# Performance work log

Measured on AMD Instinct MI355X. Metric: run time of the kernel, lower is better.

## Reference

```python
import jax, jax.numpy as jnp
import numpy as np

N_CLUSTERS = 16
N_ITERATIONS = 5
COV_INIT = 1.0


def setup_inputs() -> dict:
    key = jax.random.key(0)
    k1, k2 = jax.random.split(key)
    B, T, F, D = 8, 400, 256, 64
    data = jax.random.normal(k1, (B, T, F, D), dtype=jnp.float32)
    # Replicate init_means: per batch row, pick K random indices in [0, T),
    # offset by b*T, and gather rows of data flattened over (B,T,F).
    idx = jax.random.randint(k2, (B, N_CLUSTERS), 0, T)  # [B,K]
    idx = idx + jnp.arange(B)[:, None] * T
    flat = data.reshape(-1, D)  # [B*T*F, D]
    means = flat[idx.reshape(-1)].reshape(B, N_CLUSTERS, D)
    scale = jnp.ones((1,), dtype=jnp.float32)
    bias = jnp.zeros((1,), dtype=jnp.float32)
    return {"data": data, "means": means, "scale": scale, "bias": bias}


def _log_likelihoods(x, x2, means, var, pi):
    # x: [B,N,D], means/var: [B,K,D], pi: [B,K] -> lik: [B,K,N]
    inv = 1.0 / (var + 1e-6)
    # sum_d (x - m)^2 * inv, expanded into GEMM-friendly contractions
    dist = (jnp.einsum('bnd,bkd->bkn', x2, inv)
            - 2.0 * jnp.einsum('bnd,bkd->bkn', x, means * inv)
            + jnp.sum(means * means * inv, axis=-1)[:, :, None])
    coeff = -0.5 * jnp.sum(jnp.log(2.0 * np.pi * var), axis=-1)  # [B,K]
    return jnp.log(pi)[:, :, None] + coeff[:, :, None] - 0.5 * dist


def reference(data, means, scale, bias):
    B, T, F, D = data.shape
    K = means.shape[1]
    N = T * F
    x = data.reshape(B, N, D)
    x2 = x * x
    var = jnp.full((B, K, D), COV_INIT, dtype=data.dtype)
    pi = jnp.full((B, K), 1.0 / K, dtype=data.dtype)

    for _ in range(N_ITERATIONS):
        lik = _log_likelihoods(x, x2, means, var, pi)          # [B,K,N]
        post = jax.nn.softmax(lik, axis=1)                     # [B,K,N]
        cs = jnp.sum(post, axis=2)                             # [B,K]
        pi = cs / jnp.sum(cs, axis=1, keepdims=True)           # L1-normalized
        sx = jnp.einsum('bkn,bnd->bkd', post, x)               # [B,K,D]
        means = sx / (cs[:, :, None] + 1e-7)
        sx2 = jnp.einsum('bkn,bnd->bkd', post, x2)
        # sum_n post*(x - m)^2 = S(x^2) - 2 m S(x) + m^2 * cluster_size
        var = sx2 - 2.0 * means * sx + means * means * cs[:, :, None]
        var = var + 1e-6

    lik = _log_likelihoods(x, x2, means, var, pi)              # [B,K,N]
    lik = jnp.transpose(lik, (0, 2, 1)).reshape(B, T, F, K)
    return jax.nn.sigmoid(lik * scale[0] + bias[0])
```

## Files before the change

### kernel.cpp

```cpp
#include <hip/hip_runtime.h>
#include <math.h>

#define B_  8
#define T_  400
#define F_  256
#define D_  64
#define K_  16
#define N_  (T_*F_)
#define TILE 512
#define NBLK (N_/TILE)


__global__ void initk(const float* __restrict__ means_in,
                      float* __restrict__ means_s, float* __restrict__ var_s,
                      float* __restrict__ pi_s) {
    int i = blockIdx.x * 256 + threadIdx.x;
    if (i < B_*K_*D_) { means_s[i] = means_in[i]; var_s[i] = 1.0f; }
    if (i < B_*K_)    pi_s[i] = 1.0f / K_;
}

__global__ void prepk(const float* __restrict__ means_s, const float* __restrict__ var_s,
                      const float* __restrict__ pi_s,
                      float* __restrict__ pinv, float* __restrict__ pw,
                      float* __restrict__ pc0) {
    int bk = blockIdx.x;
    int d  = threadIdx.x;
    int idx = bk * D_ + d;
    float var = var_s[idx];
    float m   = means_s[idx];
    float inv = 1.0f / (var + 1e-6f);
    pinv[idx] = inv;
    pw[idx]   = m * inv;
    float r1 = logf(6.283185307179586f * var);
    float r2 = m * m * inv;
    #pragma unroll
    for (int off = 32; off > 0; off >>= 1) {
        r1 += __shfl_xor(r1, off);
        r2 += __shfl_xor(r2, off);
    }
    if (d == 0) pc0[bk] = logf(pi_s[bk]) - 0.5f * (r1 + r2);
}

__global__ __launch_bounds__(256, 4) void estepk(
        const float* __restrict__ xg,
        const float* __restrict__ pinv, const float* __restrict__ pw,
        const float* __restrict__ pc0,
        float* __restrict__ cs, float* __restrict__ sx, float* __restrict__ sx2) {
    __shared__ float post_lds[TILE * 16];

    const int t  = threadIdx.x;
    const int b  = blockIdx.y;
    const int n0 = blockIdx.x * TILE;

    const float4* iv4 = (const float4*)(pinv + (size_t)(b*K_*D_));
    const float4* wv4 = (const float4*)(pw   + (size_t)(b*K_*D_));

    float c0r[16];
    #pragma unroll
    for (int k = 0; k < 16; ++k) c0r[k] = pc0[b*K_ + k];

    float t1a[16], t2a[16], t1b[16], t2b[16];
    #pragma unroll
    for (int k = 0; k < 16; ++k) { t1a[k]=0.f; t2a[k]=0.f; t1b[k]=0.f; t2b[k]=0.f; }

    const float4* pa = (const float4*)(xg + ((size_t)b*N_ + n0 + t) * D_);
    const float4* pb = pa + 256 * (D_/4);

    #pragma unroll 2
    for (int c = 0; c < D_/4; ++c) {
        float4 xa = pa[c], xb = pb[c];
        float4 qa, qb;
        qa.x = xa.x*xa.x; qa.y = xa.y*xa.y; qa.z = xa.z*xa.z; qa.w = xa.w*xa.w;
        qb.x = xb.x*xb.x; qb.y = xb.y*xb.y; qb.z = xb.z*xb.z; qb.w = xb.w*xb.w;
        #pragma unroll
        for (int k = 0; k < 16; ++k) {
            float4 iv = iv4[k*16 + c];
            float4 wv = wv4[k*16 + c];
            t2a[k] = fmaf(qa.x, iv.x, fmaf(qa.y, iv.y, fmaf(qa.z, iv.z, fmaf(qa.w, iv.w, t2a[k]))));
            t1a[k] = fmaf(xa.x, wv.x, fmaf(xa.y, wv.y, fmaf(xa.z, wv.z, fmaf(xa.w, wv.w, t1a[k]))));
            t2b[k] = fmaf(qb.x, iv.x, fmaf(qb.y, iv.y, fmaf(qb.z, iv.z, fmaf(qb.w, iv.w, t2b[k]))));
            t1b[k] = fmaf(xb.x, wv.x, fmaf(xb.y, wv.y, fmaf(xb.z, wv.z, fmaf(xb.w, wv.w, t1b[k]))));
        }
    }

    {
        float lik[16]; float mx = -1e30f;
        #pragma unroll
        for (int k = 0; k < 16; ++k) { lik[k] = c0r[k] + t1a[k] - 0.5f*t2a[k]; mx = fmaxf(mx, lik[k]); }
        float s = 0.f;
        #pragma unroll
        for (int k = 0; k < 16; ++k) { lik[k] = __expf(lik[k] - mx); s += lik[k]; }
        float is = 1.0f / s;
        #pragma unroll
        for (int k = 0; k < 16; ++k) post_lds[t*16 + k] = lik[k] * is;
    }
    {
        float lik[16]; float mx = -1e30f;
        #pragma unroll
        for (int k = 0; k < 16; ++k) { lik[k] = c0r[k] + t1b[k] - 0.5f*t2b[k]; mx = fmaxf(mx, lik[k]); }
        float s = 0.f;
        #pragma unroll
        for (int k = 0; k < 16; ++k) { lik[k] = __expf(lik[k] - mx); s += lik[k]; }
        float is = 1.0f / s;
        #pragma unroll
        for (int k = 0; k < 16; ++k) post_lds[(256 + t)*16 + k] = lik[k] * is;
    }
    __syncthreads();

    const int lane = t & 63;
    const int kb   = (t >> 6) * 4;
    const int g    = lane & 15;
    const int ps   = lane >> 4;

    float sa[4][4], s2a[4][4], ca[4];
    #pragma unroll
    for (int i = 0; i < 4; ++i) {
        ca[i] = 0.f;
        #pragma unroll
        for (int j = 0; j < 4; ++j) { sa[i][j] = 0.f; s2a[i][j] = 0.f; }
    }

    const float4* xq = (const float4*)(xg + ((size_t)b*N_ + n0) * D_);

    #pragma unroll 4
    for (int n = 0; n < TILE; n += 4) {
        const int p = n + ps;
        float4 xv = xq[p*16 + g];
        float4 pv = *(const float4*)&post_lds[p*16 + kb];
        float xf[4] = {xv.x, xv.y, xv.z, xv.w};
        float pf[4] = {pv.x, pv.y, pv.z, pv.w};
        float qf[4];
        #pragma unroll
        for (int j = 0; j < 4; ++j) qf[j] = xf[j]*xf[j];
        #pragma unroll
        for (int i = 0; i < 4; ++i) {
            ca[i] += pf[i];
            #pragma unroll
            for (int j = 0; j < 4; ++j) {
                sa[i][j]  = fmaf(pf[i], xf[j], sa[i][j]);
                s2a[i][j] = fmaf(pf[i], qf[j], s2a[i][j]);
            }
        }
    }

    #pragma unroll
    for (int m = 16; m <= 32; m <<= 1) {
        #pragma unroll
        for (int i = 0; i < 4; ++i) {
            ca[i] += __shfl_xor(ca[i], m);
            #pragma unroll
            for (int j = 0; j < 4; ++j) {
                sa[i][j]  += __shfl_xor(sa[i][j],  m);
                s2a[i][j] += __shfl_xor(s2a[i][j], m);
            }
        }
    }

    if (lane < 16) {
        #pragma unroll
        for (int i = 0; i < 4; ++i) {
            #pragma unroll
            for (int j = 0; j < 4; ++j) {
                atomicAdd(&sx [((size_t)(b*K_ + kb + i))*D_ + 4*lane + j], sa[i][j]);
                atomicAdd(&sx2[((size_t)(b*K_ + kb + i))*D_ + 4*lane + j], s2a[i][j]);
            }
        }
        if (lane == 0) {
            #pragma unroll
            for (int i = 0; i < 4; ++i) atomicAdd(&cs[b*K_ + kb + i], ca[i]);
        }
    }
}

__global__ void mstepk(float* __restrict__ means_s, float* __restrict__ var_s,
                       float* __restrict__ pi_s,
                       const float* __restrict__ cs, const float* __restrict__ sx,
                       const float* __restrict__ sx2) {
    int idx = blockIdx.x * 256 + threadIdx.x;
    int b = idx >> 10;
    int k = (idx >> 6) & 15;
    int d = idx & 63;
    float csv = cs[b*K_ + k];
    float sum = 0.f;
    #pragma unroll
    for (int j = 0; j < 16; ++j) sum += cs[b*K_ + j];
    float sxv = sx[idx], sx2v = sx2[idx];
    float mean = sxv / (csv + 1e-7f);
    float var  = fmaf(mean*mean, csv, fmaf(-2.0f*mean, sxv, sx2v)) + 1e-6f;
    means_s[idx] = mean;
    var_s[idx]   = var;
    if (d == 0) pi_s[b*K_ + k] = csv / sum;
}

__global__ __launch_bounds__(256, 4) void finalk(
        const float* __restrict__ xg,
        const float* __restrict__ pinv, const float* __restrict__ pw,
        const float* __restrict__ pc0,
        const float* __restrict__ scale, const float* __restrict__ bias,
        float* __restrict__ out) {
    const int t  = threadIdx.x;
    const int b  = blockIdx.y;
    const int n0 = blockIdx.x * TILE;

    const float4* iv4 = (const float4*)(pinv + (size_t)(b*K_*D_));
    const float4* wv4 = (const float4*)(pw   + (size_t)(b*K_*D_));

    float c0r[16];
    #pragma unroll
    for (int k = 0; k < 16; ++k) c0r[k] = pc0[b*K_ + k];

    float t1a[16], t2a[16], t1b[16], t2b[16];
    #pragma unroll
    for (int k = 0; k < 16; ++k) { t1a[k]=0.f; t2a[k]=0.f; t1b[k]=0.f; t2b[k]=0.f; }

    const float4* pa = (const float4*)(xg + ((size_t)b*N_ + n0 + t) * D_);
    const float4* pb = pa + 256 * (D_/4);

    #pragma unroll 2
    for (int c = 0; c < D_/4; ++c) {
        float4 xa = pa[c], xb = pb[c];
        float4 qa, qb;
        qa.x = xa.x*xa.x; qa.y = xa.y*xa.y; qa.z = xa.z*xa.z; qa.w = xa.w*xa.w;
        qb.x = xb.x*xb.x; qb.y = xb.y*xb.y; qb.z = xb.z*xb.z; qb.w = xb.w*xb.w;
        #pragma unroll
        for (int k = 0; k < 16; ++k) {
            float4 iv = iv4[k*16 + c];
            float4 wv = wv4[k*16 + c];
            t2a[k] = fmaf(qa.x, iv.x, fmaf(qa.y, iv.y, fmaf(qa.z, iv.z, fmaf(qa.w, iv.w, t2a[k]))));
            t1a[k] = fmaf(xa.x, wv.x, fmaf(xa.y, wv.y, fmaf(xa.z, wv.z, fmaf(xa.w, wv.w, t1a[k]))));
            t2b[k] = fmaf(qb.x, iv.x, fmaf(qb.y, iv.y, fmaf(qb.z, iv.z, fmaf(qb.w, iv.w, t2b[k]))));
            t1b[k] = fmaf(xb.x, wv.x, fmaf(xb.y, wv.y, fmaf(xb.z, wv.z, fmaf(xb.w, wv.w, t1b[k]))));
        }
    }

    const float sc = scale[0], bi = bias[0];

    {
        float4* op = (float4*)(out + ((size_t)b*N_ + n0 + t) * (size_t)K_);
        #pragma unroll
        for (int q = 0; q < 4; ++q) {
            float4 o;
            float z0 = (c0r[4*q+0] + t1a[4*q+0] - 0.5f*t2a[4*q+0]) * sc + bi;
            float z1 = (c0r[4*q+1] + t1a[4*q+1] - 0.5f*t2a[4*q+1]) * sc + bi;
            float z2 = (c0r[4*q+2] + t1a[4*q+2] - 0.5f*t2a[4*q+2]) * sc + bi;
            float z3 = (c0r[4*q+3] + t1a[4*q+3] - 0.5f*t2a[4*q+3]) * sc + bi;
            o.x = 1.0f / (1.0f + __expf(-z0));
            o.y = 1.0f / (1.0f + __expf(-z1));
            o.z = 1.0f / (1.0f + __expf(-z2));
            o.w = 1.0f / (1.0f + __expf(-z3));
            op[q] = o;
        }
    }
    {
        float4* op = (float4*)(out + ((size_t)b*N_ + n0 + 256 + t) * (size_t)K_);
        #pragma unroll
        for (int q = 0; q < 4; ++q) {
            float4 o;
            float z0 = (c0r[4*q+0] + t1b[4*q+0] - 0.5f*t2b[4*q+0]) * sc + bi;
            float z1 = (c0r[4*q+1] + t1b[4*q+1] - 0.5f*t2b[4*q+1]) * sc + bi;
            float z2 = (c0r[4*q+2] + t1b[4*q+2] - 0.5f*t2b[4*q+2]) * sc + bi;
            float z3 = (c0r[4*q+3] + t1b[4*q+3] - 0.5f*t2b[4*q+3]) * sc + bi;
            o.x = 1.0f / (1.0f + __expf(-z0));
            o.y = 1.0f / (1.0f + __expf(-z1));
            o.z = 1.0f / (1.0f + __expf(-z2));
            o.w = 1.0f / (1.0f + __expf(-z3));
            op[q] = o;
        }
    }
}

extern "C" void kernel_launch(void* const* d_in, const int* in_sizes, int n_in,
                              void* d_out, int out_size, void* d_ws, size_t ws_size,
                              hipStream_t stream) {
    const float* xg       = (const float*)d_in[0];
    const float* means_in = (const float*)d_in[1];
    const float* scale    = (const float*)d_in[2];
    const float* bias     = (const float*)d_in[3];
    float* out = (float*)d_out;

    float* ws      = (float*)d_ws;
    float* means_s = ws + 0;
    float* var_s   = ws + 8192;
    float* pi_s    = ws + 16384;
    float* pinv    = ws + 16512;
    float* pw      = ws + 24704;
    float* pc0     = ws + 32896;
    float* cs      = ws + 33024;
    float* sx      = ws + 33152;
    float* sx2     = ws + 41344;

    initk<<<dim3(32), dim3(256), 0, stream>>>(means_in, means_s, var_s, pi_s);

    for (int it = 0; it < 5; ++it) {
        prepk<<<dim3(B_*K_), dim3(64), 0, stream>>>(means_s, var_s, pi_s, pinv, pw, pc0);
        hipMemsetAsync(cs, 0, (size_t)(128 + 8192 + 8192) * sizeof(float), stream);
        estepk<<<dim3(NBLK, B_), dim3(256), 0, stream>>>(xg, pinv, pw, pc0, cs, sx, sx2);
        mstepk<<<dim3(32), dim3(256), 0, stream>>>(means_s, var_s, pi_s, cs, sx, sx2);
    }
    prepk<<<dim3(B_*K_), dim3(64), 0, stream>>>(means_s, var_s, pi_s, pinv, pw, pc0);
    finalk<<<dim3(NBLK, B_), dim3(256), 0, stream>>>(xg, pinv, pw, pc0, scale, bias, out);
}
```

Before: 1.733 ms.

## Split likelihood dot products across 16 lanes with butterfly reduction and LDS params

Restructures the E-step and final likelihood so that 16 lanes each take a 4-wide slice of D for a point, with coalesced float4 loads. Per-cluster partial sums are combined by a butterfly shuffle reduction, and softmax is done with cross-lane shuffles. The per-batch parameters (mean*inv and -0.5*inv) are staged in LDS, and the tile shrinks to 256 points per block with more occupancy requested. This targets the strided per-thread row reads of x and the heavy register use of the old one-thread-per-point design. In exchange it adds shuffle traffic and launches more, smaller blocks.

```diff
diff --git a/kernel.cpp b/kernel.cpp
--- a/kernel.cpp
+++ b/kernel.cpp
@@ -7,7 +7,7 @@
 #define D_  64
 #define K_  16
 #define N_  (T_*F_)
-#define TILE 512
+#define TILE 256
 #define NBLK (N_/TILE)
 
 
@@ -21,7 +21,7 @@
 
 __global__ void prepk(const float* __restrict__ means_s, const float* __restrict__ var_s,
                       const float* __restrict__ pi_s,
-                      float* __restrict__ pinv, float* __restrict__ pw,
+                      float* __restrict__ pu, float* __restrict__ pw,
                       float* __restrict__ pc0) {
     int bk = blockIdx.x;
     int d  = threadIdx.x;
@@ -29,8 +29,8 @@
     float var = var_s[idx];
     float m   = means_s[idx];
     float inv = 1.0f / (var + 1e-6f);
-    pinv[idx] = inv;
-    pw[idx]   = m * inv;
+    pu[idx] = -0.5f * inv;
+    pw[idx] = m * inv;
     float r1 = logf(6.283185307179586f * var);
     float r2 = m * m * inv;
     #pragma unroll
@@ -41,77 +41,120 @@
     if (d == 0) pc0[bk] = logf(pi_s[bk]) - 0.5f * (r1 + r2);
 }
 
-__global__ __launch_bounds__(256, 4) void estepk(
+__device__ __forceinline__ float butterfly16(const float v[16], int g) {
+    float a[8];
+    {
+        const bool c = (g & 1);
+        #pragma unroll
+        for (int i = 0; i < 8; ++i) {
+            float send = c ? v[2*i]   : v[2*i+1];
+            float keep = c ? v[2*i+1] : v[2*i];
+            a[i] = keep + __shfl_xor(send, 1);
+        }
+    }
+    float b2[4];
+    {
+        const bool c = (g & 2);
+        #pragma unroll
+        for (int i = 0; i < 4; ++i) {
+            float send = c ? a[2*i]   : a[2*i+1];
+            float keep = c ? a[2*i+1] : a[2*i];
+            b2[i] = keep + __shfl_xor(send, 2);
+        }
+    }
+    float d2[2];
+    {
+        const bool c = (g & 4);
+        #pragma unroll
+        for (int i = 0; i < 2; ++i) {
+            float send = c ? b2[2*i]   : b2[2*i+1];
+            float keep = c ? b2[2*i+1] : b2[2*i];
+            d2[i] = keep + __shfl_xor(send, 4);
+        }
+    }
+    const bool c = (g & 8);
+    float send = c ? d2[0] : d2[1];
+    float keep = c ? d2[1] : d2[0];
+    return keep + __shfl_xor(send, 8);
+}
+
+__global__ __launch_bounds__(256, 5) void estepk(
         const float* __restrict__ xg,
-        const float* __restrict__ pinv, const float* __restrict__ pw,
+        const float* __restrict__ pu, const float* __restrict__ pw,
         const float* __restrict__ pc0,
         float* __restrict__ cs, float* __restrict__ sx, float* __restrict__ sx2) {
+    __shared__ float w_lds[K_*D_];
+    __shared__ float u_lds[K_*D_];
     __shared__ float post_lds[TILE * 16];
 
     const int t  = threadIdx.x;
     const int b  = blockIdx.y;
     const int n0 = blockIdx.x * TILE;
 
-    const float4* iv4 = (const float4*)(pinv + (size_t)(b*K_*D_));
-    const float4* wv4 = (const float4*)(pw   + (size_t)(b*K_*D_));
-
-    float c0r[16];
-    #pragma unroll
-    for (int k = 0; k < 16; ++k) c0r[k] = pc0[b*K_ + k];
-
-    float t1a[16], t2a[16], t1b[16], t2b[16];
-    #pragma unroll
-    for (int k = 0; k < 16; ++k) { t1a[k]=0.f; t2a[k]=0.f; t1b[k]=0.f; t2b[k]=0.f; }
-
-    const float4* pa = (const float4*)(xg + ((size_t)b*N_ + n0 + t) * D_);
-    const float4* pb = pa + 256 * (D_/4);
-
-    #pragma unroll 2
-    for (int c = 0; c < D_/4; ++c) {
-        float4 xa = pa[c], xb = pb[c];
-        float4 qa, qb;
-        qa.x = xa.x*xa.x; qa.y = xa.y*xa.y; qa.z = xa.z*xa.z; qa.w = xa.w*xa.w;
-        qb.x = xb.x*xb.x; qb.y = xb.y*xb.y; qb.z = xb.z*xb.z; qb.w = xb.w*xb.w;
-        #pragma unroll
-        for (int k = 0; k < 16; ++k) {
-            float4 iv = iv4[k*16 + c];
-            float4 wv = wv4[k*16 + c];
-            t2a[k] = fmaf(qa.x, iv.x, fmaf(qa.y, iv.y, fmaf(qa.z, iv.z, fmaf(qa.w, iv.w, t2a[k]))));
-            t1a[k] = fmaf(xa.x, wv.x, fmaf(xa.y, wv.y, fmaf(xa.z, wv.z, fmaf(xa.w, wv.w, t1a[k]))));
-            t2b[k] = fmaf(qb.x, iv.x, fmaf(qb.y, iv.y, fmaf(qb.z, iv.z, fmaf(qb.w, iv.w, t2b[k]))));
-            t1b[k] = fmaf(xb.x, wv.x, fmaf(xb.y, wv.y, fmaf(xb.z, wv.z, fmaf(xb.w, wv.w, t1b[k]))));
-        }
-    }
-
-    {
-        float lik[16]; float mx = -1e30f;
-        #pragma unroll
-        for (int k = 0; k < 16; ++k) { lik[k] = c0r[k] + t1a[k] - 0.5f*t2a[k]; mx = fmaxf(mx, lik[k]); }
-        float s = 0.f;
-        #pragma unroll
-        for (int k = 0; k < 16; ++k) { lik[k] = __expf(lik[k] - mx); s += lik[k]; }
-        float is = 1.0f / s;
-        #pragma unroll
-        for (int k = 0; k < 16; ++k) post_lds[t*16 + k] = lik[k] * is;
-    }
-    {
-        float lik[16]; float mx = -1e30f;
-        #pragma unroll
-        for (int k = 0; k < 16; ++k) { lik[k] = c0r[k] + t1b[k] - 0.5f*t2b[k]; mx = fmaxf(mx, lik[k]); }
-        float s = 0.f;
-        #pragma unroll
-        for (int k = 0; k < 16; ++k) { lik[k] = __expf(lik[k] - mx); s += lik[k]; }
-        float is = 1.0f / s;
-        #pragma unroll
-        for (int k = 0; k < 16; ++k) post_lds[(256 + t)*16 + k] = lik[k] * is;
-    }
-    __syncthreads();
+    for (int i = t; i < K_*D_; i += 256) {
+        w_lds[i] = pw[b*K_*D_ + i];
+        u_lds[i] = pu[b*K_*D_ + i];
+    }
 
     const int lane = t & 63;
-    const int kb   = (t >> 6) * 4;
     const int g    = lane & 15;
     const int ps   = lane >> 4;
-
+    const int w    = t >> 6;
+
+    const float c0_lane = pc0[b*K_ + g];
+    const float4* xq = (const float4*)(xg + ((size_t)b*N_ + n0) * D_);
+    const float4* w4 = (const float4*)w_lds;
+    const float4* u4 = (const float4*)u_lds;
+    __syncthreads();
+
+    #pragma unroll 2
+    for (int s = 0; s < 8; ++s) {
+        const int p0 = w*64 + s*8 + ps;
+        const int p1 = p0 + 4;
+        float4 xv0 = xq[p0*16 + g];
+        float4 xv1 = xq[p1*16 + g];
+        float4 q0, q1;
+        q0.x = xv0.x*xv0.x; q0.y = xv0.y*xv0.y; q0.z = xv0.z*xv0.z; q0.w = xv0.w*xv0.w;
+        q1.x = xv1.x*xv1.x; q1.y = xv1.y*xv1.y; q1.z = xv1.z*xv1.z; q1.w = xv1.w*xv1.w;
+
+        float v0[16], v1[16];
+        #pragma unroll
+        for (int k = 0; k < 16; ++k) {
+            const float4 wv = w4[k*16 + g];
+            const float4 uv = u4[k*16 + g];
+            float r0 = xv0.x*wv.x;       r0 = fmaf(q0.x, uv.x, r0);
+            r0 = fmaf(xv0.y, wv.y, r0);  r0 = fmaf(q0.y, uv.y, r0);
+            r0 = fmaf(xv0.z, wv.z, r0);  r0 = fmaf(q0.z, uv.z, r0);
+            r0 = fmaf(xv0.w, wv.w, r0);  r0 = fmaf(q0.w, uv.w, r0);
+            v0[k] = r0;
+            float r1 = xv1.x*wv.x;       r1 = fmaf(q1.x, uv.x, r1);
+            r1 = fmaf(xv1.y, wv.y, r1);  r1 = fmaf(q1.y, uv.y, r1);
+            r1 = fmaf(xv1.z, wv.z, r1);  r1 = fmaf(q1.z, uv.z, r1);
+            r1 = fmaf(xv1.w, wv.w, r1);  r1 = fmaf(q1.w, uv.w, r1);
+            v1[k] = r1;
+        }
+
+        #pragma unroll
+        for (int pp = 0; pp < 2; ++pp) {
+            float lik = (pp ? butterfly16(v1, g) : butterfly16(v0, g)) + c0_lane;
+            float mx = lik;
+            mx = fmaxf(mx, __shfl_xor(mx, 1));
+            mx = fmaxf(mx, __shfl_xor(mx, 2));
+            mx = fmaxf(mx, __shfl_xor(mx, 4));
+            mx = fmaxf(mx, __shfl_xor(mx, 8));
+            float ex = __expf(lik - mx);
+            float sm = ex;
+            sm += __shfl_xor(sm, 1);
+            sm += __shfl_xor(sm, 2);
+            sm += __shfl_xor(sm, 4);
+            sm += __shfl_xor(sm, 8);
+            const int p = pp ? p1 : p0;
+            post_lds[p*16 + g] = ex / sm;
+        }
+    }
+    __syncthreads();
+
+    const int kb = w * 4;
     float sa[4][4], s2a[4][4], ca[4];
     #pragma unroll
     for (int i = 0; i < 4; ++i) {
@@ -119,8 +162,6 @@
         #pragma unroll
         for (int j = 0; j < 4; ++j) { sa[i][j] = 0.f; s2a[i][j] = 0.f; }
     }
-
-    const float4* xq = (const float4*)(xg + ((size_t)b*N_ + n0) * D_);
 
     #pragma unroll 4
     for (int n = 0; n < TILE; n += 4) {
@@ -192,80 +233,70 @@
     if (d == 0) pi_s[b*K_ + k] = csv / sum;
 }
 
-__global__ __launch_bounds__(256, 4) void finalk(
+__global__ __launch_bounds__(256, 5) void finalk(
         const float* __restrict__ xg,
-        const float* __restrict__ pinv, const float* __restrict__ pw,
+        const float* __restrict__ pu, const float* __restrict__ pw,
         const float* __restrict__ pc0,
         const float* __restrict__ scale, const float* __restrict__ bias,
         float* __restrict__ out) {
+    __shared__ float w_lds[K_*D_];
+    __shared__ float u_lds[K_*D_];
+
     const int t  = threadIdx.x;
     const int b  = blockIdx.y;
     const int n0 = blockIdx.x * TILE;
 
-    const float4* iv4 = (const float4*)(pinv + (size_t)(b*K_*D_));
-    const float4* wv4 = (const float4*)(pw   + (size_t)(b*K_*D_));
-
-    float c0r[16];
-    #pragma unroll
-    for (int k = 0; k < 16; ++k) c0r[k] = pc0[b*K_ + k];
-
-    float t1a[16], t2a[16], t1b[16], t2b[16];
-    #pragma unroll
-    for (int k = 0; k < 16; ++k) { t1a[k]=0.f; t2a[k]=0.f; t1b[k]=0.f; t2b[k]=0.f; }
-
-    const float4* pa = (const float4*)(xg + ((size_t)b*N_ + n0 + t) * D_);
-    const float4* pb = pa + 256 * (D_/4);
+    for (int i = t; i < K_*D_; i += 256) {
+        w_lds[i] = pw[b*K_*D_ + i];
+        u_lds[i] = pu[b*K_*D_ + i];
+    }
+
+    const int lane = t & 63;
+    const int g    = lane & 15;
+    const int ps   = lane >> 4;
+    const int w    = t >> 6;
+
+    const float c0_lane = pc0[b*K_ + g];
+    const float sc = scale[0], bi = bias[0];
+    const float4* xq = (const float4*)(xg + ((size_t)b*N_ + n0) * D_);
+    const float4* w4 = (const float4*)w_lds;
+    const float4* u4 = (const float4*)u_lds;
+    float* outb = out + ((size_t)b*N_ + n0) * (size_t)K_;
+    __syncthreads();
 
     #pragma unroll 2
-    for (int c = 0; c < D_/4; ++c) {
-        float4 xa = pa[c], xb = pb[c];
-        float4 qa, qb;
-        qa.x = xa.x*xa.x; qa.y = xa.y*xa.y; qa.z = xa.z*xa.z; qa.w = xa.w*xa.w;
-        qb.x = xb.x*xb.x; qb.y = xb.y*xb.y; qb.z = xb.z*xb.z; qb.w = xb.w*xb.w;
+    for (int s = 0; s < 8; ++s) {
+        const int p0 = w*64 + s*8 + ps;
+        const int p1 = p0 + 4;
+        float4 xv0 = xq[p0*16 + g];
+        float4 xv1 = xq[p1*16 + g];
+        float4 q0, q1;
+        q0.x = xv0.x*xv0.x; q0.y = xv0.y*xv0.y; q0.z = xv0.z*xv0.z; q0.w = xv0.w*xv0.w;
+        q1.x = xv1.x*xv1.x; q1.y = xv1.y*xv1.y; q1.z = xv1.z*xv1.z; q1.w = xv1.w*xv1.w;
+
+        float v0[16], v1[16];
         #pragma unroll
         for (int k = 0; k < 16; ++k) {
-            float4 iv = iv4[k*16 + c];
-            float4 wv = wv4[k*16 + c];
-            t2a[k] = fmaf(qa.x, iv.x, fmaf(qa.y, iv.y, fmaf(qa.z, iv.z, fmaf(qa.w, iv.w, t2a[k]))));
-            t1a[k] = fmaf(xa.x, wv.x, fmaf(xa.y, wv.y, fmaf(xa.z, wv.z, fmaf(xa.w, wv.w, t1a[k]))));
-            t2b[k] = fmaf(qb.x, iv.x, fmaf(qb.y, iv.y, fmaf(qb.z, iv.z, fmaf(qb.w, iv.w, t2b[k]))));
-            t1b[k] = fmaf(xb.x, wv.x, fmaf(xb.y, wv.y, fmaf(xb.z, wv.z, fmaf(xb.w, wv.w, t1b[k]))));
-        }
-    }
-
-    const float sc = scale[0], bi = bias[0];
-
-    {
-        float4* op = (float4*)(out + ((size_t)b*N_ + n0 + t) * (size_t)K_);
-        #pragma unroll
-        for (int q = 0; q < 4; ++q) {
-            float4 o;
-            float z0 = (c0r[4*q+0] + t1a[4*q+0] - 0.5f*t2a[4*q+0]) * sc + bi;
-            float z1 = (c0r[4*q+1] + t1a[4*q+1] - 0.5f*t2a[4*q+1]) * sc + bi;
-            float z2 = (c0r[4*q+2] + t1a[4*q+2] - 0.5f*t2a[4*q+2]) * sc + bi;
-            float z3 = (c0r[4*q+3] + t1a[4*q+3] - 0.5f*t2a[4*q+3]) * sc + bi;
-            o.x = 1.0f / (1.0f + __expf(-z0));
-            o.y = 1.0f / (1.0f + __expf(-z1));
-            o.z = 1.0f / (1.0f + __expf(-z2));
-            o.w = 1.0f / (1.0f + __expf(-z3));
-            op[q] = o;
-        }
-    }
-    {
-        float4* op = (float4*)(out + ((size_t)b*N_ + n0 + 256 + t) * (size_t)K_);
-        #pragma unroll
-        for (int q = 0; q < 4; ++q) {
-            float4 o;
-            float z0 = (c0r[4*q+0] + t1b[4*q+0] - 0.5f*t2b[4*q+0]) * sc + bi;
-            float z1 = (c0r[4*q+1] + t1b[4*q+1] - 0.5f*t2b[4*q+1]) * sc + bi;
-            float z2 = (c0r[4*q+2] + t1b[4*q+2] - 0.5f*t2b[4*q+2]) * sc + bi;
-            float z3 = (c0r[4*q+3] + t1b[4*q+3] - 0.5f*t2b[4*q+3]) * sc + bi;
-            o.x = 1.0f / (1.0f + __expf(-z0));
-            o.y = 1.0f / (1.0f + __expf(-z1));
-            o.z = 1.0f / (1.0f + __expf(-z2));
-            o.w = 1.0f / (1.0f + __expf(-z3));
-            op[q] = o;
-        }
+            const float4 wv = w4[k*16 + g];
+            const float4 uv = u4[k*16 + g];
+            float r0 = xv0.x*wv.x;       r0 = fmaf(q0.x, uv.x, r0);
+            r0 = fmaf(xv0.y, wv.y, r0);  r0 = fmaf(q0.y, uv.y, r0);
+            r0 = fmaf(xv0.z, wv.z, r0);  r0 = fmaf(q0.z, uv.z, r0);
+            r0 = fmaf(xv0.w, wv.w, r0);  r0 = fmaf(q0.w, uv.w, r0);
+            v0[k] = r0;
+            float r1 = xv1.x*wv.x;       r1 = fmaf(q1.x, uv.x, r1);
+            r1 = fmaf(xv1.y, wv.y, r1);  r1 = fmaf(q1.y, uv.y, r1);
+            r1 = fmaf(xv1.z, wv.z, r1);  r1 = fmaf(q1.z, uv.z, r1);
+            r1 = fmaf(xv1.w, wv.w, r1);  r1 = fmaf(q1.w, uv.w, r1);
+            v1[k] = r1;
+        }
+
+        float lik0 = butterfly16(v0, g) + c0_lane;
+        float lik1 = butterfly16(v1, g) + c0_lane;
+        float z0 = fmaf(lik0, sc, bi);
+        float z1 = fmaf(lik1, sc, bi);
+        outb[(size_t)p0*K_ + g] = 1.0f / (1.0f + __expf(-z0));
+        outb[(size_t)p1*K_ + g] = 1.0f / (1.0f + __expf(-z1));
     }
 }
 
@@ -282,7 +313,7 @@
     float* means_s = ws + 0;
     float* var_s   = ws + 8192;
     float* pi_s    = ws + 16384;
-    float* pinv    = ws + 16512;
+    float* pu      = ws + 16512;
     float* pw      = ws + 24704;
     float* pc0     = ws + 32896;
     float* cs      = ws + 33024;
@@ -292,11 +323,11 @@
     initk<<<dim3(32), dim3(256), 0, stream>>>(means_in, means_s, var_s, pi_s);
 
     for (int it = 0; it < 5; ++it) {
-        prepk<<<dim3(B_*K_), dim3(64), 0, stream>>>(means_s, var_s, pi_s, pinv, pw, pc0);
+        prepk<<<dim3(B_*K_), dim3(64), 0, stream>>>(means_s, var_s, pi_s, pu, pw, pc0);
         hipMemsetAsync(cs, 0, (size_t)(128 + 8192 + 8192) * sizeof(float), stream);
-        estepk<<<dim3(NBLK, B_), dim3(256), 0, stream>>>(xg, pinv, pw, pc0, cs, sx, sx2);
+        estepk<<<dim3(NBLK, B_), dim3(256), 0, stream>>>(xg, pu, pw, pc0, cs, sx, sx2);
         mstepk<<<dim3(32), dim3(256), 0, stream>>>(means_s, var_s, pi_s, cs, sx, sx2);
     }
-    prepk<<<dim3(B_*K_), dim3(64), 0, stream>>>(means_s, var_s, pi_s, pinv, pw, pc0);
-    finalk<<<dim3(NBLK, B_), dim3(256), 0, stream>>>(xg, pinv, pw, pc0, scale, bias, out);
-}
+    prepk<<<dim3(B_*K_), dim3(64), 0, stream>>>(means_s, var_s, pi_s, pu, pw, pc0);
+    finalk<<<dim3(NBLK, B_), dim3(256), 0, stream>>>(xg, pu, pw, pc0, scale, bias, out);
+}
```

Measured after the change: 5.356 ms. 209% more time.
